# Kernel tuning notes

Measured on AMD Instinct MI355X. Metric: run time of the kernel, lower is better.

The kernel has to match this reference:

```python
import jax, jax.numpy as jnp
import numpy as np

B, S, D, H = 2, 2048, 1024, 16
DK = D // H  # 64


def setup_inputs() -> dict:
    key = jax.random.key(0)
    ks = jax.random.split(key, 9)
    scale = 1.0 / np.sqrt(D)
    inp = {
        "q": jax.random.normal(ks[0], (B, S, D), dtype=jnp.float32),
        "k": jax.random.normal(ks[1], (B, S, D), dtype=jnp.float32),
        "v": jax.random.normal(ks[2], (B, S, D), dtype=jnp.float32),
        "Wq": jax.random.normal(ks[3], (D, D), dtype=jnp.float32) * scale,
        "bq": jax.random.normal(ks[4], (D,), dtype=jnp.float32) * scale,
        "Wk": jax.random.normal(ks[5], (D, D), dtype=jnp.float32) * scale,
        "bk": jax.random.normal(ks[6], (D,), dtype=jnp.float32) * scale,
        "Wv": jax.random.normal(ks[7], (D, D), dtype=jnp.float32) * scale,
        "bv": jax.random.normal(ks[8], (D,), dtype=jnp.float32) * scale,
        "mask": jnp.tril(jnp.ones((S, S), dtype=jnp.int32))[None, None],  # [1,1,S,S] causal
    }
    return inp


def reference(q, k, v, Wq, bq, Wk, bk, Wv, bv, mask):
    b, s, d = q.shape
    # QKV projections -> [B, H, S, DK]
    qh = (q @ Wq + bq).reshape(b, s, H, DK).transpose(0, 2, 1, 3)
    kh = (k @ Wk + bk).reshape(b, s, H, DK).transpose(0, 2, 1, 3)
    vh = (v @ Wv + bv).reshape(b, s, H, DK).transpose(0, 2, 1, 3)
    # scores [B, H, Sq, Sk]
    scores = jnp.einsum("bhqd,bhkd->bhqk", qh, kh) / jnp.sqrt(jnp.float32(DK))
    scores = jnp.where(mask == 0, jnp.float32(-1e9), scores)
    attn = jax.nn.softmax(scores, axis=-1)  # dropout is identity at inference
    out = jnp.einsum("bhqk,bhkd->bhqd", attn, vh)
    return out.transpose(0, 2, 1, 3).reshape(b, s, d)
```

## Files before the change

### kernel.cpp

```cpp
#include <hip/hip_runtime.h>
#include <hip/hip_bf16.h>

#define D_MODEL 1024
#define SEQ 2048
#define NH 16
#define DKH 64
#define MROWS 4096

typedef __attribute__((ext_vector_type(8))) short bf16x8;
typedef __attribute__((ext_vector_type(4))) float f32x4;
typedef __attribute__((ext_vector_type(4))) int int4v;

__device__ inline short f2bf(float f) {
    __hip_bfloat16 h = __float2bfloat16(f);
    return __builtin_bit_cast(short, h);
}

#define GLOAD16(gsrc, ldst)                                                     \
    __builtin_amdgcn_global_load_lds(                                           \
        (const __attribute__((address_space(1))) void*)(gsrc),                  \
        (__attribute__((address_space(3))) void*)(ldst), 16, 0, 0)

__global__ __launch_bounds__(256) void prep_kernel(
    const float* __restrict__ q, const float* __restrict__ k,
    const float* __restrict__ v,
    const float* __restrict__ Wq, const float* __restrict__ Wk,
    const float* __restrict__ Wv,
    short* __restrict__ aqkv, short* __restrict__ Wt) {
    __shared__ float tile[32][33];
    const int bx = blockIdx.x;
    if (bx < 6144) {
        const int z = bx >> 11;
        const int blk = bx & 2047;
        const float* src = (z == 0) ? q : (z == 1) ? k : v;
        short* dst = aqkv + (size_t)z * MROWS * D_MODEL;
        const size_t i = ((size_t)blk * 256 + threadIdx.x) * 8;
        float4 f0 = *(const float4*)(src + i);
        float4 f1 = *(const float4*)(src + i + 4);
        bf16x8 p;
        p[0] = f2bf(f0.x); p[1] = f2bf(f0.y); p[2] = f2bf(f0.z); p[3] = f2bf(f0.w);
        p[4] = f2bf(f1.x); p[5] = f2bf(f1.y); p[6] = f2bf(f1.z); p[7] = f2bf(f1.w);
        *(bf16x8*)(dst + i) = p;
    } else {
        int b = bx - 6144;
        const int z = b >> 10; b &= 1023;
        const float* W = (z == 0) ? Wq : (z == 1) ? Wk : Wv;
        short* dst = Wt + (size_t)z * D_MODEL * D_MODEL;
        const int n0 = (b & 31) * 32, k0 = (b >> 5) * 32;
        const int tx = threadIdx.x & 31, ty = threadIdx.x >> 5;
        for (int i = 0; i < 4; ++i)
            tile[ty + 8 * i][tx] = W[(size_t)(k0 + ty + 8 * i) * D_MODEL + n0 + tx];
        __syncthreads();
        for (int i = 0; i < 4; ++i)
            dst[(size_t)(n0 + ty + 8 * i) * D_MODEL + k0 + tx] = f2bf(tile[tx][ty + 8 * i]);
    }
}

__global__ __launch_bounds__(256) void proj_kernel(
    const short* __restrict__ aqkv, const short* __restrict__ Wt,
    const float* __restrict__ bq, const float* __restrict__ bk, const float* __restrict__ bv,
    short* __restrict__ qh, short* __restrict__ kh, short* __restrict__ vT) {
    __shared__ short sA[128 * 64];
    __shared__ short sB[128 * 64];

    const int z = blockIdx.z;
    const short* A = aqkv + (size_t)z * MROWS * D_MODEL;
    const short* B = Wt + (size_t)z * D_MODEL * D_MODEL;
    const float* bias = (z == 0) ? bq : (z == 1) ? bk : bv;
    short* dst = (z == 0) ? qh : (z == 1) ? kh : vT;

    const int m0 = blockIdx.y * 128;
    const int n0 = blockIdx.x * 128;
    const int tid = threadIdx.x;
    const int lane = tid & 63;
    const int w = tid >> 6;
    const int wr = w >> 1, wc = w & 1;
    const int lg = lane >> 4, ll = lane & 15;

    const int c0 = w * 4;
    const int srow = lane >> 3;
    const int scol = ((lane & 7) ^ srow) << 3;

    const int cs0 = ((lg * 16) ^ ((ll & 7) << 4)) >> 1;
    const int cs1 = ((64 + lg * 16) ^ ((ll & 7) << 4)) >> 1;

    f32x4 acc[4][4] = {};

    for (int kt = 0; kt < D_MODEL / 64; ++kt) {
        const int kk0 = kt * 64;
        __syncthreads();
        for (int i = 0; i < 4; ++i) {
            const int c = c0 + i;
            const int row = c * 8 + srow;
            GLOAD16(A + (size_t)(m0 + row) * D_MODEL + kk0 + scol, &sA[c * 512]);
            GLOAD16(B + (size_t)(n0 + row) * D_MODEL + kk0 + scol, &sB[c * 512]);
        }
        __syncthreads();

        bf16x8 af[4][2], bfr[4][2];
        for (int i = 0; i < 4; ++i) {
            const int rb = (wr * 64 + i * 16 + ll) * 64;
            af[i][0] = *(const bf16x8*)&sA[rb + cs0];
            af[i][1] = *(const bf16x8*)&sA[rb + cs1];
        }
        for (int j = 0; j < 4; ++j) {
            const int rb = (wc * 64 + j * 16 + ll) * 64;
            bfr[j][0] = *(const bf16x8*)&sB[rb + cs0];
            bfr[j][1] = *(const bf16x8*)&sB[rb + cs1];
        }
        for (int kk = 0; kk < 2; ++kk)
            for (int i = 0; i < 4; ++i)
                for (int j = 0; j < 4; ++j)
                    acc[i][j] = __builtin_amdgcn_mfma_f32_16x16x32_bf16(af[i][kk], bfr[j][kk], acc[i][j], 0, 0, 0);
    }

    for (int j = 0; j < 4; ++j) {
        const int n = n0 + wc * 64 + j * 16 + ll;
        const float bn = bias[n];
        const int h = n >> 6, dk = n & 63;
        for (int i = 0; i < 4; ++i) {
            for (int rr = 0; rr < 4; ++rr) {
                const int m = m0 + wr * 64 + i * 16 + lg * 4 + rr;
                float val = acc[i][j][rr] + bn;
                if (z == 0) val *= 0.125f;
                const int b = m >> 11, s = m & 2047;
                size_t idx;
                if (z < 2) idx = (((size_t)(b * NH + h)) * SEQ + s) * DKH + dk;
                else       idx = (((size_t)(b * NH + h)) * DKH + dk) * SEQ + s;
                dst[idx] = f2bf(val);
            }
        }
    }
}

__global__ __launch_bounds__(256) void attn_kernel(
    const short* __restrict__ qh, const short* __restrict__ kh,
    const short* __restrict__ vT, float* __restrict__ out) {
    __shared__ short sK[2][64 * 64];
    __shared__ short sV[2][64 * 64];
    __shared__ short sP[4][16 * 72];

    const int flat = blockIdx.x;
    const int qt = 31 - (flat >> 5);
    const int bh = flat & 31;
    const int q0 = qt * 64;
    const int tid = threadIdx.x;
    const int w = tid >> 6;
    const int lane = tid & 63;
    const int lg = lane >> 4, ll = lane & 15;
    const int b = bh >> 4, h = bh & 15;

    const short* kbase = kh + (size_t)bh * SEQ * DKH;
    const short* vbase = vT + (size_t)bh * DKH * SEQ;

    const int srow = lane >> 3;
    const int scol = ((lane & 7) ^ srow) << 3;
    const int cs0 = ((lg * 16) ^ ((ll & 7) << 4)) >> 1;
    const int cs1 = ((64 + lg * 16) ^ ((ll & 7) << 4)) >> 1;

#define ASTAGE(buf, t)                                                          \
    for (int c_ = 2 * w; c_ < 2 * w + 2; ++c_) {                                \
        const int row_ = c_ * 8 + srow;                                         \
        GLOAD16(kbase + (size_t)((t) * 64 + row_) * DKH + scol, &sK[buf][c_ * 512]); \
        GLOAD16(vbase + (size_t)row_ * SEQ + (t) * 64 + scol, &sV[buf][c_ * 512]);   \
    }

    bf16x8 qf[2];
    {
        const short* src = qh + (((size_t)bh * SEQ) + q0 + w * 16 + ll) * DKH + lg * 8;
        qf[0] = *(const bf16x8*)(src);
        qf[1] = *(const bf16x8*)(src + 32);
    }

    f32x4 acc[4] = {};
    float l_i[4] = {0.f, 0.f, 0.f, 0.f};

    const int ntiles = qt + 1;
    int cur = 0;
    ASTAGE(0, 0);
    __syncthreads();

    for (int t = 0; t < ntiles; ++t) {
        if (t + 1 < ntiles) ASTAGE(cur ^ 1, t + 1);

        f32x4 sc[4] = {};
        __builtin_amdgcn_s_setprio(1);
        for (int j = 0; j < 4; ++j) {
            const int rb = (j * 16 + ll) * 64;
            bf16x8 kf0 = *(const bf16x8*)&sK[cur][rb + cs0];
            bf16x8 kf1 = *(const bf16x8*)&sK[cur][rb + cs1];
            sc[j] = __builtin_amdgcn_mfma_f32_16x16x32_bf16(qf[0], kf0, sc[j], 0, 0, 0);
            sc[j] = __builtin_amdgcn_mfma_f32_16x16x32_bf16(qf[1], kf1, sc[j], 0, 0, 0);
        }
        __builtin_amdgcn_s_setprio(0);

        if (t == ntiles - 1) {
            const int k0 = t * 64;
            for (int j = 0; j < 4; ++j) {
                const int key = k0 + j * 16 + ll;
                for (int r = 0; r < 4; ++r) {
                    const int qrow = q0 + w * 16 + lg * 4 + r;
                    if (key > qrow) sc[j][r] = -1e30f;
                }
            }
        }

        for (int j = 0; j < 4; ++j)
            for (int r = 0; r < 4; ++r)
                sc[j][r] = __expf(sc[j][r]);
        for (int r = 0; r < 4; ++r)
            l_i[r] += (sc[0][r] + sc[1][r]) + (sc[2][r] + sc[3][r]);

        for (int j = 0; j < 4; ++j)
            for (int r = 0; r < 4; ++r)
                sP[w][(lg * 4 + r) * 72 + j * 16 + ll] = f2bf(sc[j][r]);

        bf16x8 pf0 = *(const bf16x8*)&sP[w][ll * 72 + lg * 8];
        bf16x8 pf1 = *(const bf16x8*)&sP[w][ll * 72 + lg * 8 + 32];

        __builtin_amdgcn_s_setprio(1);
        for (int j = 0; j < 4; ++j) {
            const int rb = (j * 16 + ll) * 64;
            bf16x8 vf0 = *(const bf16x8*)&sV[cur][rb + cs0];
            bf16x8 vf1 = *(const bf16x8*)&sV[cur][rb + cs1];
            acc[j] = __builtin_amdgcn_mfma_f32_16x16x32_bf16(pf0, vf0, acc[j], 0, 0, 0);
            acc[j] = __builtin_amdgcn_mfma_f32_16x16x32_bf16(pf1, vf1, acc[j], 0, 0, 0);
        }
        __builtin_amdgcn_s_setprio(0);

        __syncthreads();
        cur ^= 1;
    }

    for (int r = 0; r < 4; ++r) {
        float ts = l_i[r];
        ts += __shfl_xor(ts, 1);
        ts += __shfl_xor(ts, 2);
        ts += __shfl_xor(ts, 4);
        ts += __shfl_xor(ts, 8);
        l_i[r] = ts;
    }
    for (int j = 0; j < 4; ++j) {
        for (int r = 0; r < 4; ++r) {
            const int qrow = q0 + w * 16 + lg * 4 + r;
            out[((size_t)(b * SEQ + qrow)) * D_MODEL + h * DKH + j * 16 + ll] =
                acc[j][r] / l_i[r];
        }
    }
#undef ASTAGE
}

extern "C" void kernel_launch(void* const* d_in, const int* in_sizes, int n_in,
                              void* d_out, int out_size, void* d_ws, size_t ws_size,
                              hipStream_t stream) {
    const float* q  = (const float*)d_in[0];
    const float* k  = (const float*)d_in[1];
    const float* v  = (const float*)d_in[2];
    const float* Wq = (const float*)d_in[3];
    const float* bq = (const float*)d_in[4];
    const float* Wk = (const float*)d_in[5];
    const float* bk = (const float*)d_in[6];
    const float* Wv = (const float*)d_in[7];
    const float* bv = (const float*)d_in[8];
    float* out = (float*)d_out;

    short* aqkv = (short*)d_ws;
    short* Wt = aqkv + (size_t)3 * MROWS * D_MODEL;
    short* qh = Wt + (size_t)3 * D_MODEL * D_MODEL;
    short* kh = qh + (size_t)MROWS * D_MODEL;
    short* vT = kh + (size_t)MROWS * D_MODEL;

    hipLaunchKernelGGL(prep_kernel, dim3(9216), dim3(256), 0, stream,
                       q, k, v, Wq, Wk, Wv, aqkv, Wt);
    hipLaunchKernelGGL(proj_kernel, dim3(8, 32, 3), dim3(256), 0, stream,
                       aqkv, Wt, bq, bk, bv, qh, kh, vT);
    hipLaunchKernelGGL(attn_kernel, dim3(1024), dim3(256), 0, stream, qh, kh, vT, out);
}
```

Measured before the change: 217.6 us.

## Double-buffer projection GEMM LDS tiles and remap blocks across XCDs

Restructures the projection GEMM to use two LDS buffers with a K-step of 32, so the async global-to-LDS load of the next tile is issued before computing on the current one, removing one barrier per iteration. The launch grid is flattened to 768 blocks and a block-index permutation groups related tiles per XCD to improve L2 reuse. The risk is that the smaller K-step doubles loop iterations and barrier count, and the swizzle changes bank behaviour.

```diff
diff --git a/kernel.cpp b/kernel.cpp
--- a/kernel.cpp
+++ b/kernel.cpp
@@ -60,59 +60,61 @@
     const short* __restrict__ aqkv, const short* __restrict__ Wt,
     const float* __restrict__ bq, const float* __restrict__ bk, const float* __restrict__ bv,
     short* __restrict__ qh, short* __restrict__ kh, short* __restrict__ vT) {
-    __shared__ short sA[128 * 64];
-    __shared__ short sB[128 * 64];
-
-    const int z = blockIdx.z;
+    __shared__ short sA[2][128 * 32];
+    __shared__ short sB[2][128 * 32];
+
+    const int flat = blockIdx.x;
+    const int nf = (flat & 7) * 96 + (flat >> 3);
+    const int z = nf >> 8;
+    const int rem = nf & 255;
+    const int m0 = (rem >> 3) * 128;
+    const int n0 = (rem & 7) * 128;
+
     const short* A = aqkv + (size_t)z * MROWS * D_MODEL;
     const short* B = Wt + (size_t)z * D_MODEL * D_MODEL;
     const float* bias = (z == 0) ? bq : (z == 1) ? bk : bv;
     short* dst = (z == 0) ? qh : (z == 1) ? kh : vT;
 
-    const int m0 = blockIdx.y * 128;
-    const int n0 = blockIdx.x * 128;
     const int tid = threadIdx.x;
     const int lane = tid & 63;
     const int w = tid >> 6;
     const int wr = w >> 1, wc = w & 1;
     const int lg = lane >> 4, ll = lane & 15;
 
-    const int c0 = w * 4;
-    const int srow = lane >> 3;
-    const int scol = ((lane & 7) ^ srow) << 3;
-
-    const int cs0 = ((lg * 16) ^ ((ll & 7) << 4)) >> 1;
-    const int cs1 = ((64 + lg * 16) ^ ((ll & 7) << 4)) >> 1;
+    const int srow = lane >> 2;
+    const int scol = ((lane & 3) ^ (srow & 3)) << 3;
+
+    const int cs = (lg * 8) ^ ((ll & 3) << 3);
 
     f32x4 acc[4][4] = {};
 
-    for (int kt = 0; kt < D_MODEL / 64; ++kt) {
-        const int kk0 = kt * 64;
+#define STAGE(buf, kt)                                                          \
+    for (int c_ = 2 * w; c_ < 2 * w + 2; ++c_) {                                \
+        const int row_ = c_ * 16 + srow;                                        \
+        GLOAD16(A + (size_t)(m0 + row_) * D_MODEL + (kt) * 32 + scol, &sA[buf][c_ * 512]); \
+        GLOAD16(B + (size_t)(n0 + row_) * D_MODEL + (kt) * 32 + scol, &sB[buf][c_ * 512]); \
+    }
+
+    STAGE(0, 0);
+    __syncthreads();
+    int cur = 0;
+
+    for (int kt = 0; kt < 32; ++kt) {
+        if (kt + 1 < 32) STAGE(cur ^ 1, kt + 1);
+
+        bf16x8 af[4], bfr[4];
+        for (int i = 0; i < 4; ++i)
+            af[i] = *(const bf16x8*)&sA[cur][(wr * 64 + i * 16 + ll) * 32 + cs];
+        for (int j = 0; j < 4; ++j)
+            bfr[j] = *(const bf16x8*)&sB[cur][(wc * 64 + j * 16 + ll) * 32 + cs];
+        for (int i = 0; i < 4; ++i)
+            for (int j = 0; j < 4; ++j)
+                acc[i][j] = __builtin_amdgcn_mfma_f32_16x16x32_bf16(af[i], bfr[j], acc[i][j], 0, 0, 0);
+
         __syncthreads();
-        for (int i = 0; i < 4; ++i) {
-            const int c = c0 + i;
-            const int row = c * 8 + srow;
-            GLOAD16(A + (size_t)(m0 + row) * D_MODEL + kk0 + scol, &sA[c * 512]);
-            GLOAD16(B + (size_t)(n0 + row) * D_MODEL + kk0 + scol, &sB[c * 512]);
-        }
-        __syncthreads();
-
-        bf16x8 af[4][2], bfr[4][2];
-        for (int i = 0; i < 4; ++i) {
-            const int rb = (wr * 64 + i * 16 + ll) * 64;
-            af[i][0] = *(const bf16x8*)&sA[rb + cs0];
-            af[i][1] = *(const bf16x8*)&sA[rb + cs1];
-        }
-        for (int j = 0; j < 4; ++j) {
-            const int rb = (wc * 64 + j * 16 + ll) * 64;
-            bfr[j][0] = *(const bf16x8*)&sB[rb + cs0];
-            bfr[j][1] = *(const bf16x8*)&sB[rb + cs1];
-        }
-        for (int kk = 0; kk < 2; ++kk)
-            for (int i = 0; i < 4; ++i)
-                for (int j = 0; j < 4; ++j)
-                    acc[i][j] = __builtin_amdgcn_mfma_f32_16x16x32_bf16(af[i][kk], bfr[j][kk], acc[i][j], 0, 0, 0);
-    }
+        cur ^= 1;
+    }
+#undef STAGE
 
     for (int j = 0; j < 4; ++j) {
         const int n = n0 + wc * 64 + j * 16 + ll;
@@ -272,7 +274,7 @@
 
     hipLaunchKernelGGL(prep_kernel, dim3(9216), dim3(256), 0, stream,
                        q, k, v, Wq, Wk, Wv, aqkv, Wt);
-    hipLaunchKernelGGL(proj_kernel, dim3(8, 32, 3), dim3(256), 0, stream,
+    hipLaunchKernelGGL(proj_kernel, dim3(768), dim3(256), 0, stream,
                        aqkv, Wt, bq, bk, bv, qh, kh, vT);
     hipLaunchKernelGGL(attn_kernel, dim3(1024), dim3(256), 0, stream, qh, kh, vT, out);
 }
```

New measurement: 216.1 us. Within noise of the previous version (-0.7%).
